# Kernel tuning notes

Hardware: AMD Instinct MI355X
Metric: run time of the kernel (lower is better)

Reference implementation:

```python
import jax, jax.numpy as jnp
import numpy as np

NUM_MOVIES = 100000
MOVIE_FEAT = 128
USER_FEAT = 128
BATCH = 16384
N_NBRS = 50
D0, D1, D2 = 256, 256, 128  # layer_dims


def setup_inputs() -> dict:
    key = jax.random.key(0)
    ks = jax.random.split(key, 16)
    inp = {
        "users": jax.random.normal(ks[0], (BATCH, USER_FEAT), jnp.float32),
        "pos_movies": jax.random.normal(ks[1], (BATCH, MOVIE_FEAT), jnp.float32),
        "neg_movies": jax.random.normal(ks[2], (BATCH, MOVIE_FEAT), jnp.float32),
        "user_ids": jax.random.randint(ks[3], (BATCH,), 0, BATCH),
        "pos_movie_ids": jax.random.randint(ks[4], (BATCH,), 0, NUM_MOVIES),
        "neg_movie_ids": jax.random.randint(ks[5], (BATCH,), 0, NUM_MOVIES),
        "nbr_ids": jax.random.randint(ks[6], (BATCH, N_NBRS), 0, NUM_MOVIES),
        # learned params / buffers
        "movie_table": jax.random.normal(ks[7], (NUM_MOVIES, MOVIE_FEAT), jnp.float32),
        "Wu": jax.random.normal(ks[8], (USER_FEAT, D0), jnp.float32) * (1.0 / np.sqrt(USER_FEAT)),
        "bu": jnp.zeros((D0,), jnp.float32),
        "Wm": jax.random.normal(ks[9], (MOVIE_FEAT, D0), jnp.float32) * (1.0 / np.sqrt(MOVIE_FEAT)),
        "bm": jnp.zeros((D0,), jnp.float32),
        "W1": jax.random.normal(ks[10], (D0, D1), jnp.float32) * (1.0 / np.sqrt(D0)),
        "b1": jnp.zeros((D1,), jnp.float32),
        "W2": jax.random.normal(ks[11], (D1, D2), jnp.float32) * (1.0 / np.sqrt(D1)),
        "b2": jnp.zeros((D2,), jnp.float32),
    }
    return inp


def reference(users, pos_movies, neg_movies, user_ids, pos_movie_ids, neg_movie_ids,
              nbr_ids, movie_table, Wu, bu, Wm, bm, W1, b1, W2, b2):
    # user_projection / movie_projection
    user_emb = users @ Wu + bu                      # [B, D0]
    movie_emb = movie_table @ Wm + bm               # [N, D0]
    pos_emb = movie_emb[pos_movie_ids]              # [B, D0]
    neg_emb = movie_emb[neg_movie_ids]              # [B, D0]
    # vectorized replacement of the per-user neighbor gather + mean loop
    nbr_mean = jnp.mean(movie_emb[nbr_ids], axis=1)  # [B, N_NBRS, D0] -> [B, D0]
    user_emb = user_emb + nbr_mean
    x = jnp.stack([user_emb, pos_emb, neg_emb], axis=0)  # [3, B, D0]
    x = jax.nn.relu(x @ W1 + b1)
    x = jax.nn.relu(x @ W2 + b2)
    return (x[0], x[1], x[2])
```

## Files before the change

kernel.cpp:

```cpp
#include <hip/hip_runtime.h>
#include <hip/hip_bf16.h>

#define BATCH_N   16384
#define FEAT      128
#define NNBR      50
#define NUM_MOVIES_N 100000

typedef short  short8  __attribute__((ext_vector_type(8)));
typedef float  floatx4 __attribute__((ext_vector_type(4)));
typedef unsigned int u32;

__device__ __forceinline__ __hip_bfloat16 f2bf(float x) { return __float2bfloat16(x); }
__device__ __forceinline__ float bfb2f(short s) {
  union { u32 u; float f; } c; c.u = ((u32)(unsigned short)s) << 16; return c.f;
}

__device__ __forceinline__ void gld16(const __hip_bfloat16* g, __hip_bfloat16* l) {
  __builtin_amdgcn_global_load_lds(
      (const __attribute__((address_space(1))) u32*)g,
      (__attribute__((address_space(3))) u32*)l, 16, 0, 0);
}

__device__ __forceinline__ floatx4 mfma16(short8 a, short8 b, floatx4 c) {
  return __builtin_amdgcn_mfma_f32_16x16x32_bf16(a, b, c, 0, 0, 0);
}

__global__ __launch_bounds__(256) void conv_table(
    const float* __restrict__ t, __hip_bfloat16* __restrict__ tb) {
  size_t i = ((size_t)blockIdx.x * 256 + threadIdx.x) * 8;
  float4 v0 = *(const float4*)(t + i);
  float4 v1 = *(const float4*)(t + i + 4);
  __hip_bfloat16 o[8];
  o[0] = f2bf(v0.x); o[1] = f2bf(v0.y); o[2] = f2bf(v0.z); o[3] = f2bf(v0.w);
  o[4] = f2bf(v1.x); o[5] = f2bf(v1.y); o[6] = f2bf(v1.z); o[7] = f2bf(v1.w);
  *(short8*)(tb + i) = *(short8*)o;
}

__global__ __launch_bounds__(256) void prep_kernel(
    const float* __restrict__ Wu, const float* __restrict__ Wm,
    const float* __restrict__ W1, const float* __restrict__ W2,
    const float* __restrict__ bu, const float* __restrict__ bm,
    __hip_bfloat16* __restrict__ WcatT, __hip_bfloat16* __restrict__ WmT,
    __hip_bfloat16* __restrict__ W1T,  __hip_bfloat16* __restrict__ W2T,
    float* __restrict__ bc) {
  int idx = blockIdx.x * 256 + threadIdx.x;
  int n = idx & 255, k = idx >> 8;
  float v = (k < 128) ? Wu[k * 256 + n] : Wm[(k - 128) * 256 + n];
  WcatT[n * 256 + k] = f2bf(v);
  W1T[n * 256 + k]   = f2bf(W1[k * 256 + n]);
  if (k < 128) WmT[n * 128 + k] = f2bf(Wm[k * 256 + n]);
  if (idx < 32768) {
    int k2 = idx >> 7, n2 = idx & 127;
    W2T[n2 * 256 + k2] = f2bf(W2[k2 * 128 + n2]);
  }
  if (idx < 256) bc[idx] = bu[idx] + bm[idx];
}

__global__ __launch_bounds__(256) void gather_user(
    const float* __restrict__ users, const int* __restrict__ nbr_ids,
    const __hip_bfloat16* __restrict__ tb, __hip_bfloat16* __restrict__ A_user) {
  int row  = (blockIdx.x << 2) + (threadIdx.x >> 6);
  int lane = threadIdx.x & 63;
  int quad = lane >> 4, sl = lane & 15;
  const int* nb = nbr_ids + row * NNBR;
  float acc[8] = {0.f, 0.f, 0.f, 0.f, 0.f, 0.f, 0.f, 0.f};
  #pragma unroll
  for (int it = 0; it < 13; ++it) {
    int j = it * 4 + quad;
    if (j < NNBR) {
      int id = nb[j];
      short8 v = *(const short8*)(tb + (size_t)id * FEAT + sl * 8);
      #pragma unroll
      for (int e = 0; e < 8; ++e) acc[e] += bfb2f(v[e]);
    }
  }
  __hip_bfloat16 o[8];
  #pragma unroll
  for (int e = 0; e < 8; ++e) {
    float v = acc[e];
    v += __shfl_xor(v, 16, 64);
    v += __shfl_xor(v, 32, 64);
    o[e] = f2bf(v * (1.f / NNBR));
  }
  if (quad == 0)
    *(short8*)(A_user + (size_t)row * 256 + 128 + sl * 8) = *(short8*)o;
  float2 uv = ((const float2*)(users + (size_t)row * FEAT))[lane];
  __hip_bfloat162 t0; t0.x = f2bf(uv.x); t0.y = f2bf(uv.y);
  ((__hip_bfloat162*)(A_user + (size_t)row * 256))[lane] = t0;
}

template <int K0, int NCOL, bool RELU, bool TOGLB>
__device__ __forceinline__ void run_layer(
    const __hip_bfloat16* Ain, __hip_bfloat16* Bst,
    const __hip_bfloat16* __restrict__ W, const float* __restrict__ bias,
    __hip_bfloat16* Olds, float* __restrict__ Oglb,
    int t, int wm, int wn, int quad, int lrow, long m0) {
  constexpr int KK = K0 / 32;
  constexpr int JN = NCOL / 32;
  floatx4 acc[JN] = {};
  for (int kc = 0; kc < KK; ++kc) {
    const int k0 = kc * 32;
    __syncthreads();
    #pragma unroll
    for (int i = 0; i < NCOL / 64; ++i) {
      int c = t + i * 256;
      int n = c >> 2, q = c & 3;
      gld16(W + (size_t)n * K0 + k0 + ((q ^ ((n >> 1) & 3)) << 3),
            Bst + (c << 3));
    }
    __syncthreads();
    int r = wm * 16 + lrow;
    short8 af = *(const short8*)&Ain[r * K0 + ((((k0 >> 3) + quad) ^ (r & 7)) << 3)];
    #pragma unroll
    for (int j = 0; j < JN; ++j) {
      int n = wn * (NCOL / 2) + j * 16 + lrow;
      short8 bf = *(const short8*)&Bst[n * 32 + ((quad ^ ((n >> 1) & 3)) << 3)];
      acc[j] = mfma16(af, bf, acc[j]);
    }
  }
  __syncthreads();
  #pragma unroll
  for (int j = 0; j < JN; ++j) {
    int col = wn * (NCOL / 2) + j * 16 + lrow;
    float bv = bias[col];
    #pragma unroll
    for (int r = 0; r < 4; ++r) {
      int row = wm * 16 + quad * 4 + r;
      float v = acc[j][r] + bv;
      if (RELU) v = fmaxf(v, 0.f);
      if (TOGLB) {
        Oglb[(m0 + row) * 128 + col] = v;
      } else {
        int ch = col >> 3;
        Olds[row * 256 + (((ch ^ (row & 7)) << 3) | (col & 7))] = f2bf(v);
      }
    }
  }
}

__global__ __launch_bounds__(256, 4) void fused_mlp(
    const __hip_bfloat16* __restrict__ A_user,
    const __hip_bfloat16* __restrict__ tb,
    const int* __restrict__ pos_ids, const int* __restrict__ neg_ids,
    const __hip_bfloat16* __restrict__ WcatT,
    const __hip_bfloat16* __restrict__ WmT,
    const __hip_bfloat16* __restrict__ W1T,
    const __hip_bfloat16* __restrict__ W2T,
    const float* __restrict__ bc, const float* __restrict__ bmv,
    const float* __restrict__ b1, const float* __restrict__ b2,
    float* __restrict__ out) {
  __shared__ __hip_bfloat16 A_lds[32 * 256];
  __shared__ __hip_bfloat16 E_lds[32 * 256];

  const int t    = threadIdx.x;
  const int lane = t & 63, wid = t >> 6;
  const int wm   = wid & 1, wn = wid >> 1;
  const int quad = lane >> 4, lrow = lane & 15;
  const int bx   = blockIdx.x;
  const int s    = bx % 3;
  const long m0  = (long)(bx / 3) * 32;

  if (s == 0) {
    #pragma unroll
    for (int i = 0; i < 4; ++i) {
      int c = t + i * 256;
      int r = c >> 5, kq = c & 31;
      gld16(A_user + ((size_t)(m0 + r) << 8) + ((kq ^ (r & 7)) << 3),
            A_lds + (c << 3));
    }
  } else {
    const int* ids = (s == 1) ? pos_ids : neg_ids;
    #pragma unroll
    for (int i = 0; i < 2; ++i) {
      int c = t + i * 256;
      int r = c >> 4, kq = c & 15;
      int id = ids[m0 + r];
      gld16(tb + ((size_t)id << 7) + ((kq ^ (r & 7)) << 3),
            A_lds + (c << 3));
    }
  }

  if (s == 0)
    run_layer<256, 256, false, false>(A_lds, E_lds, WcatT, bc, E_lds, nullptr,
                                      t, wm, wn, quad, lrow, m0);
  else
    run_layer<128, 256, false, false>(A_lds, E_lds, WmT, bmv, E_lds, nullptr,
                                      t, wm, wn, quad, lrow, m0);

  run_layer<256, 256, true, false>(E_lds, A_lds, W1T, b1, A_lds, nullptr,
                                   t, wm, wn, quad, lrow, m0);

  run_layer<256, 128, true, true>(A_lds, E_lds, W2T, b2, nullptr,
                                  out + (size_t)s * BATCH_N * 128,
                                  t, wm, wn, quad, lrow, m0);
}

extern "C" void kernel_launch(void* const* d_in, const int* in_sizes, int n_in,
                              void* d_out, int out_size, void* d_ws, size_t ws_size,
                              hipStream_t stream) {
  const float* users   = (const float*)d_in[0];
  const int*   pos_ids = (const int*)d_in[4];
  const int*   neg_ids = (const int*)d_in[5];
  const int*   nbr_ids = (const int*)d_in[6];
  const float* table   = (const float*)d_in[7];
  const float* Wu = (const float*)d_in[8];
  const float* bu = (const float*)d_in[9];
  const float* Wm = (const float*)d_in[10];
  const float* bm = (const float*)d_in[11];
  const float* W1 = (const float*)d_in[12];
  const float* b1 = (const float*)d_in[13];
  const float* W2 = (const float*)d_in[14];
  const float* b2 = (const float*)d_in[15];
  float* out = (float*)d_out;

  char* p = (char*)d_ws;
  auto carve = [&](size_t bytes) { char* r = p; p += (bytes + 255) & ~(size_t)255; return r; };
  __hip_bfloat16* tb     = (__hip_bfloat16*)carve((size_t)NUM_MOVIES_N * FEAT * 2);
  __hip_bfloat16* WcatT  = (__hip_bfloat16*)carve(256 * 256 * 2);
  __hip_bfloat16* WmT    = (__hip_bfloat16*)carve(256 * 128 * 2);
  __hip_bfloat16* W1T    = (__hip_bfloat16*)carve(256 * 256 * 2);
  __hip_bfloat16* W2T    = (__hip_bfloat16*)carve(128 * 256 * 2);
  float*          bc     = (float*)carve(256 * 4);
  __hip_bfloat16* A_user = (__hip_bfloat16*)carve((size_t)BATCH_N * 256 * 2);

  conv_table<<<NUM_MOVIES_N * FEAT / (256 * 8), 256, 0, stream>>>(table, tb);
  prep_kernel<<<256, 256, 0, stream>>>(Wu, Wm, W1, W2, bu, bm,
                                       WcatT, WmT, W1T, W2T, bc);
  gather_user<<<BATCH_N / 4, 256, 0, stream>>>(users, nbr_ids, tb, A_user);
  fused_mlp<<<dim3(3 * BATCH_N / 32), 256, 0, stream>>>(
      A_user, tb, pos_ids, neg_ids, WcatT, WmT, W1T, W2T,
      bc, bm, b1, b2, out);
}
```

Baseline: 220.0 us.

## Split fused MLP into per-layer register-resident-weight GEMM kernels

Replaces the single fused three-layer kernel, which staged weights through LDS on every k-chunk with many barriers, with four separate GEMM launches. Each wave now holds a 32-column weight slice in registers and streams A rows straight from global memory with double-buffered register loads, so no LDS and no syncs are needed. The cost is writing and re-reading bf16 intermediates E and H through global memory (about 50 MB of extra traffic), plus higher register pressure and more launches.

```diff
diff --git a/kernel.cpp b/kernel.cpp
--- a/kernel.cpp
+++ b/kernel.cpp
@@ -13,12 +13,6 @@
 __device__ __forceinline__ __hip_bfloat16 f2bf(float x) { return __float2bfloat16(x); }
 __device__ __forceinline__ float bfb2f(short s) {
   union { u32 u; float f; } c; c.u = ((u32)(unsigned short)s) << 16; return c.f;
-}
-
-__device__ __forceinline__ void gld16(const __hip_bfloat16* g, __hip_bfloat16* l) {
-  __builtin_amdgcn_global_load_lds(
-      (const __attribute__((address_space(1))) u32*)g,
-      (__attribute__((address_space(3))) u32*)l, 16, 0, 0);
 }
 
 __device__ __forceinline__ floatx4 mfma16(short8 a, short8 b, floatx4 c) {
@@ -89,110 +83,72 @@
   ((__hip_bfloat162*)(A_user + (size_t)row * 256))[lane] = t0;
 }
 
-template <int K0, int NCOL, bool RELU, bool TOGLB>
-__device__ __forceinline__ void run_layer(
-    const __hip_bfloat16* Ain, __hip_bfloat16* Bst,
-    const __hip_bfloat16* __restrict__ W, const float* __restrict__ bias,
-    __hip_bfloat16* Olds, float* __restrict__ Oglb,
-    int t, int wm, int wn, int quad, int lrow, long m0) {
+template <int K0, bool GATHER, bool RELU, bool OUTF32, int NTOT, int IT>
+__global__ __launch_bounds__(256) void gemm_bv(
+    const __hip_bfloat16* __restrict__ Asrc,
+    const int* __restrict__ pos_ids, const int* __restrict__ neg_ids,
+    const __hip_bfloat16* __restrict__ Wt, const float* __restrict__ bias,
+    float* __restrict__ Cf, __hip_bfloat16* __restrict__ Cb) {
   constexpr int KK = K0 / 32;
-  constexpr int JN = NCOL / 32;
-  floatx4 acc[JN] = {};
-  for (int kc = 0; kc < KK; ++kc) {
-    const int k0 = kc * 32;
-    __syncthreads();
-    #pragma unroll
-    for (int i = 0; i < NCOL / 64; ++i) {
-      int c = t + i * 256;
-      int n = c >> 2, q = c & 3;
-      gld16(W + (size_t)n * K0 + k0 + ((q ^ ((n >> 1) & 3)) << 3),
-            Bst + (c << 3));
-    }
-    __syncthreads();
-    int r = wm * 16 + lrow;
-    short8 af = *(const short8*)&Ain[r * K0 + ((((k0 >> 3) + quad) ^ (r & 7)) << 3)];
-    #pragma unroll
-    for (int j = 0; j < JN; ++j) {
-      int n = wn * (NCOL / 2) + j * 16 + lrow;
-      short8 bf = *(const short8*)&Bst[n * 32 + ((quad ^ ((n >> 1) & 3)) << 3)];
-      acc[j] = mfma16(af, bf, acc[j]);
-    }
-  }
-  __syncthreads();
-  #pragma unroll
-  for (int j = 0; j < JN; ++j) {
-    int col = wn * (NCOL / 2) + j * 16 + lrow;
-    float bv = bias[col];
+  const int lane = threadIdx.x & 63, wid = threadIdx.x >> 6;
+  const int quad = lane >> 4, lrow = lane & 15;
+  const int c0 = blockIdx.y * 128 + wid * 32;
+  const long mbase = (long)blockIdx.x * (16 * IT);
+
+  short8 bfr[2][KK];
+  #pragma unroll
+  for (int j = 0; j < 2; ++j)
+    #pragma unroll
+    for (int kc = 0; kc < KK; ++kc)
+      bfr[j][kc] = *(const short8*)(Wt + (size_t)(c0 + j * 16 + lrow) * K0 +
+                                    kc * 32 + quad * 8);
+  const float bv0 = bias[c0 + lrow];
+  const float bv1 = bias[c0 + 16 + lrow];
+
+  short8 abuf[2][KK];
+  auto loadA = [&](int it, short8* dst) {
+    long m = mbase + it * 16 + lrow;
+    const __hip_bfloat16* rp;
+    if (GATHER) {
+      int id = (m < BATCH_N) ? pos_ids[m] : neg_ids[m - BATCH_N];
+      rp = Asrc + (size_t)id * K0;
+    } else {
+      rp = Asrc + (size_t)m * K0;
+    }
+    #pragma unroll
+    for (int kc = 0; kc < KK; ++kc)
+      dst[kc] = *(const short8*)(rp + kc * 32 + quad * 8);
+  };
+
+  loadA(0, abuf[0]);
+  #pragma unroll
+  for (int it = 0; it < IT; ++it) {
+    if (it + 1 < IT) loadA(it + 1, abuf[(it + 1) & 1]);
+    const short8* af = abuf[it & 1];
+    floatx4 p0a = {}, p0b = {}, p1a = {}, p1b = {};
+    #pragma unroll
+    for (int kc = 0; kc < KK; kc += 2) {
+      p0a = mfma16(af[kc],     bfr[0][kc],     p0a);
+      p1a = mfma16(af[kc],     bfr[1][kc],     p1a);
+      p0b = mfma16(af[kc + 1], bfr[0][kc + 1], p0b);
+      p1b = mfma16(af[kc + 1], bfr[1][kc + 1], p1b);
+    }
+    floatx4 a0 = p0a + p0b, a1 = p1a + p1b;
+    long m0 = mbase + it * 16;
     #pragma unroll
     for (int r = 0; r < 4; ++r) {
-      int row = wm * 16 + quad * 4 + r;
-      float v = acc[j][r] + bv;
-      if (RELU) v = fmaxf(v, 0.f);
-      if (TOGLB) {
-        Oglb[(m0 + row) * 128 + col] = v;
+      long row = m0 + quad * 4 + r;
+      float v0 = a0[r] + bv0, v1 = a1[r] + bv1;
+      if (RELU) { v0 = fmaxf(v0, 0.f); v1 = fmaxf(v1, 0.f); }
+      if (OUTF32) {
+        Cf[row * NTOT + c0 + lrow]      = v0;
+        Cf[row * NTOT + c0 + 16 + lrow] = v1;
       } else {
-        int ch = col >> 3;
-        Olds[row * 256 + (((ch ^ (row & 7)) << 3) | (col & 7))] = f2bf(v);
+        Cb[row * NTOT + c0 + lrow]      = f2bf(v0);
+        Cb[row * NTOT + c0 + 16 + lrow] = f2bf(v1);
       }
     }
   }
-}
-
-__global__ __launch_bounds__(256, 4) void fused_mlp(
-    const __hip_bfloat16* __restrict__ A_user,
-    const __hip_bfloat16* __restrict__ tb,
-    const int* __restrict__ pos_ids, const int* __restrict__ neg_ids,
-    const __hip_bfloat16* __restrict__ WcatT,
-    const __hip_bfloat16* __restrict__ WmT,
-    const __hip_bfloat16* __restrict__ W1T,
-    const __hip_bfloat16* __restrict__ W2T,
-    const float* __restrict__ bc, const float* __restrict__ bmv,
-    const float* __restrict__ b1, const float* __restrict__ b2,
-    float* __restrict__ out) {
-  __shared__ __hip_bfloat16 A_lds[32 * 256];
-  __shared__ __hip_bfloat16 E_lds[32 * 256];
-
-  const int t    = threadIdx.x;
-  const int lane = t & 63, wid = t >> 6;
-  const int wm   = wid & 1, wn = wid >> 1;
-  const int quad = lane >> 4, lrow = lane & 15;
-  const int bx   = blockIdx.x;
-  const int s    = bx % 3;
-  const long m0  = (long)(bx / 3) * 32;
-
-  if (s == 0) {
-    #pragma unroll
-    for (int i = 0; i < 4; ++i) {
-      int c = t + i * 256;
-      int r = c >> 5, kq = c & 31;
-      gld16(A_user + ((size_t)(m0 + r) << 8) + ((kq ^ (r & 7)) << 3),
-            A_lds + (c << 3));
-    }
-  } else {
-    const int* ids = (s == 1) ? pos_ids : neg_ids;
-    #pragma unroll
-    for (int i = 0; i < 2; ++i) {
-      int c = t + i * 256;
-      int r = c >> 4, kq = c & 15;
-      int id = ids[m0 + r];
-      gld16(tb + ((size_t)id << 7) + ((kq ^ (r & 7)) << 3),
-            A_lds + (c << 3));
-    }
-  }
-
-  if (s == 0)
-    run_layer<256, 256, false, false>(A_lds, E_lds, WcatT, bc, E_lds, nullptr,
-                                      t, wm, wn, quad, lrow, m0);
-  else
-    run_layer<128, 256, false, false>(A_lds, E_lds, WmT, bmv, E_lds, nullptr,
-                                      t, wm, wn, quad, lrow, m0);
-
-  run_layer<256, 256, true, false>(E_lds, A_lds, W1T, b1, A_lds, nullptr,
-                                   t, wm, wn, quad, lrow, m0);
-
-  run_layer<256, 128, true, true>(A_lds, E_lds, W2T, b2, nullptr,
-                                  out + (size_t)s * BATCH_N * 128,
-                                  t, wm, wn, quad, lrow, m0);
 }
 
 extern "C" void kernel_launch(void* const* d_in, const int* in_sizes, int n_in,
@@ -222,12 +178,24 @@
   __hip_bfloat16* W2T    = (__hip_bfloat16*)carve(128 * 256 * 2);
   float*          bc     = (float*)carve(256 * 4);
   __hip_bfloat16* A_user = (__hip_bfloat16*)carve((size_t)BATCH_N * 256 * 2);
+  __hip_bfloat16* E      = (__hip_bfloat16*)carve((size_t)3 * BATCH_N * 256 * 2);
+  __hip_bfloat16* H      = (__hip_bfloat16*)carve((size_t)3 * BATCH_N * 256 * 2);
 
   conv_table<<<NUM_MOVIES_N * FEAT / (256 * 8), 256, 0, stream>>>(table, tb);
   prep_kernel<<<256, 256, 0, stream>>>(Wu, Wm, W1, W2, bu, bm,
                                        WcatT, WmT, W1T, W2T, bc);
   gather_user<<<BATCH_N / 4, 256, 0, stream>>>(users, nbr_ids, tb, A_user);
-  fused_mlp<<<dim3(3 * BATCH_N / 32), 256, 0, stream>>>(
-      A_user, tb, pos_ids, neg_ids, WcatT, WmT, W1T, W2T,
-      bc, bm, b1, b2, out);
-}
+
+  gemm_bv<256, false, false, false, 256, 4>
+      <<<dim3(BATCH_N / 64, 2), 256, 0, stream>>>(
+          A_user, nullptr, nullptr, WcatT, bc, nullptr, E);
+  gemm_bv<128, true, false, false, 256, 4>
+      <<<dim3(2 * BATCH_N / 64, 2), 256, 0, stream>>>(
+          tb, pos_ids, neg_ids, WmT, bm, nullptr, E + (size_t)BATCH_N * 256);
+  gemm_bv<256, false, true, false, 256, 4>
+      <<<dim3(3 * BATCH_N / 64, 2), 256, 0, stream>>>(
+          E, nullptr, nullptr, W1T, b1, nullptr, H);
+  gemm_bv<256, false, true, true, 128, 4>
+      <<<dim3(3 * BATCH_N / 64, 1), 256, 0, stream>>>(
+          H, nullptr, nullptr, W2T, b2, out, nullptr);
+}
```

Measured after the change: 251.1 us. +14.1%, slower.
